# Kernel optimization log

Measured on AMD Instinct MI355X. Metric: run time of the kernel, lower is better.

The kernel has to match this reference:

```python
import jax, jax.numpy as jnp
import numpy as np

B, S, D, H, E, K = 4, 1024, 1024, 16, 8, 2
DH = D // H
FF = 4 * D  # expert hidden dim
EPS = 1e-5


def _layernorm(x, g, b):
    mu = jnp.mean(x, axis=-1, keepdims=True)
    var = jnp.mean(jnp.square(x - mu), axis=-1, keepdims=True)
    return (x - mu) / jnp.sqrt(var + EPS) * g + b


def setup_inputs() -> dict:
    key = jax.random.key(0)
    ks = jax.random.split(key, 16)
    s = 0.02
    return {
        "x": jax.random.normal(ks[0], (B, S, D), jnp.float32),
        "mask": jnp.ones((B, S), jnp.int32),
        "ln1_g": jnp.ones((D,), jnp.float32),
        "ln1_b": jnp.zeros((D,), jnp.float32),
        "ln2_g": jnp.ones((D,), jnp.float32),
        "ln2_b": jnp.zeros((D,), jnp.float32),
        "wq": jax.random.normal(ks[1], (D, D), jnp.float32) * s,
        "bq": jnp.zeros((D,), jnp.float32),
        "wk": jax.random.normal(ks[2], (D, D), jnp.float32) * s,
        "bk": jnp.zeros((D,), jnp.float32),
        "wv": jax.random.normal(ks[3], (D, D), jnp.float32) * s,
        "bv": jnp.zeros((D,), jnp.float32),
        "wo": jax.random.normal(ks[4], (D, D), jnp.float32) * s,
        "bo": jnp.zeros((D,), jnp.float32),
        "w_router": jax.random.normal(ks[5], (D, E), jnp.float32) * s,
        "b_router": jnp.zeros((E,), jnp.float32),
        "w1": jax.random.normal(ks[6], (E, D, FF), jnp.float32) * s,
        "b1": jnp.zeros((E, FF), jnp.float32),
        "w2": jax.random.normal(ks[7], (E, FF, D), jnp.float32) * s,
        "b2": jnp.zeros((E, D), jnp.float32),
    }


def _forward(x, mask, ln1_g, ln1_b, ln2_g, ln2_b, wq, bq, wk, bk, wv, bv,
             wo, bo, w_router, b_router, w1, b1, w2, b2):
    scale = DH ** -0.5
    # --- attention sub-block (pre-LN) ---
    xn = _layernorm(x, ln1_g, ln1_b)
    q = (xn @ wq + bq).reshape(B, S, H, DH).transpose(0, 2, 1, 3)  # [B,H,S,DH]
    k = (xn @ wk + bk).reshape(B, S, H, DH).transpose(0, 2, 1, 3)
    v = (xn @ wv + bv).reshape(B, S, H, DH).transpose(0, 2, 1, 3)
    scores = jnp.einsum('bhqd,bhkd->bhqk', q, k) * scale
    scores = jnp.where(mask[:, None, None, :] == 0, -jnp.inf, scores)
    attn = jax.nn.softmax(scores, axis=-1)
    ao = jnp.einsum('bhqk,bhkd->bhqd', attn, v)
    ao = ao.transpose(0, 2, 1, 3).reshape(B, S, D) @ wo + bo
    x = x + ao  # dropout is identity in eval
    # --- MoE sub-block ---
    xn2 = _layernorm(x, ln2_g, ln2_b)
    logits = xn2 @ w_router + b_router          # [B,S,E]
    top_v, top_i = jax.lax.top_k(logits, K)     # [B,S,K]
    probs = jax.nn.softmax(top_v, axis=-1)      # softmax over top-k logits
    # dense combine weight per expert: sum_k prob_k * onehot(idx_k)
    combine = jnp.sum(jax.nn.one_hot(top_i, E, dtype=xn2.dtype) * probs[..., None], axis=-2)  # [B,S,E]
    h = jax.nn.gelu(jnp.einsum('bsd,edh->ebsh', xn2, w1) + b1[:, None, None, :], approximate=False)
    eo = jnp.einsum('ebsh,ehd->ebsd', h, w2) + b2[:, None, None, :]   # [E,B,S,D]
    moe_out = jnp.einsum('bse,ebsd->bsd', combine, eo)
    return x + moe_out


def reference(x, mask, ln1_g, ln1_b, ln2_g, ln2_b, wq, bq, wk, bk, wv, bv,
              wo, bo, w_router, b_router, w1, b1, w2, b2):
    return _forward(x, mask, ln1_g, ln1_b, ln2_g, ln2_b, wq, bq, wk, bk, wv,
                    bv, wo, bo, w_router, b_router, w1, b1, w2, b2)
```

## Files before the change

### kernel.cpp

```cpp
#include <hip/hip_runtime.h>
#include <hip/hip_bf16.h>
#include <cmath>

typedef __hip_bfloat16 bf16;
typedef float f32x4 __attribute__((ext_vector_type(4)));
typedef int   i32x4 __attribute__((ext_vector_type(4)));

#define DEV static __device__ __forceinline__

constexpr int BB   = 4;
constexpr int SS   = 1024;
constexpr int DM   = 1024;
constexpr int HH   = 16;
constexpr int DHD  = 64;
constexpr int NEXP = 8;
constexpr int FFD  = 4096;
constexpr int NTOK = BB*SS;
constexpr int CAP  = NTOK*2 + NEXP*128;

DEV float bf2f(unsigned short u){ union{unsigned int i; float f;} z; z.i=((unsigned int)u)<<16; return z.f; }
DEV unsigned short f2bf(float f){ bf16 h = __float2bfloat16(f); return __builtin_bit_cast(unsigned short, h); }

DEV void stage16(const void* g, void* lds_base_uniform) {
  __builtin_amdgcn_global_load_lds(
      (const __attribute__((address_space(1))) void*)g,
      (__attribute__((address_space(3))) void*)lds_base_uniform,
      16, 0, 0);
}

template<int BM,int BN,int EPI,bool EXPERT,bool GATHER,bool OUT_SLOT,int NPASS=1,int ZMODE=0>
__global__ __launch_bounds__((BM/64)*(BN/64)*64)
void et_gemm(const bf16* __restrict__ A, const bf16* __restrict__ Bt, void* __restrict__ Cout,
             const float* __restrict__ bias, const float* __restrict__ res,
             int Kdim, int lda, int ldb, int ldc,
             long abs_, long bbs_, long cbs_, float scale,
             const int* __restrict__ pad_off, const int* __restrict__ slots,
             long psA, long psB, float* __restrict__ Cf, int bias_zs)
{
  constexpr int WN = BN/64, WM = BM/64, NW = WM*WN;
  constexpr int CA = (BM/16)/NW, CB = (BN/16)/NW;
  const int tid = threadIdx.x, wid = tid>>6, lane = tid&63;

  const int gx = gridDim.x, gy = gridDim.y;
  const long nwg = (long)gx*gy*gridDim.z;
  long lin = blockIdx.x + (long)gx*(blockIdx.y + (long)gy*blockIdx.z);
  {
    const long q = nwg >> 3, r = nwg & 7;
    const long xcd = lin & 7, idx = lin >> 3;
    lin = (xcd < r ? xcd*(q+1) : r*(q+1) + (xcd-r)*q) + idx;
  }
  const int bxi = (int)(lin % gx);
  const long rem = lin / gx;
  const int byi = (int)(rem % gy);
  const int bzi = (int)(rem / gy);

  const int row0 = bxi*BM, col0 = byi*BN;
  const int z = bzi;
  int off0 = 0;
  if constexpr (EXPERT) {
    off0 = pad_off[z];
    const int rows = pad_off[z+1] - off0;
    if (row0 >= rows) return;
  }
  long coff;
  if constexpr (ZMODE==2) {
    A  += (long)z*SS*SS;
    Bt += (long)z*DHD*SS;
    coff = (long)(z>>4)*SS*DM + (long)(z&15)*64;
  } else {
    if constexpr (!EXPERT) A += (size_t)z * abs_;
    Bt += (size_t)z * bbs_;
    coff = (long)z*cbs_;
  }
  const long bofs = (long)z * bias_zs;

  const int sr = lane>>2;
  const int sk = (lane&3)*8;

  long arow[CA];
  #pragma unroll
  for (int i=0;i<CA;i++){
    const int r = (wid + i*NW)*16 + sr;
    if constexpr (GATHER)      arow[i] = slots[off0 + row0 + r];
    else if constexpr (EXPERT) arow[i] = off0 + row0 + r;
    else                       arow[i] = row0 + r;
  }
  int brow[CB];
  #pragma unroll
  for (int i=0;i<CB;i++) brow[i] = col0 + (wid + i*NW)*16 + sr;

  const int wm = wid / WN, wn = wid % WN;
  const int fr = lane & 15, fg = lane >> 4;

  f32x4 acc[4][4];
  #pragma unroll
  for (int m=0;m<4;m++)
    #pragma unroll
    for (int n=0;n<4;n++) acc[m][n] = (f32x4)(0.f);

  if constexpr (NPASS==3) {
    __shared__ __align__(16) bf16 As[2][2][BM*32];
    __shared__ __align__(16) bf16 Bs[2][2][BN*32];
    auto STG = [&](int buf, int kt) {
      #pragma unroll
      for (int i=0;i<CA;i++){
        stage16(A +        arow[i]*(long)lda + kt + sk, (void*)&As[buf][0][(wid + i*NW)*512]);
        stage16(A + psA +  arow[i]*(long)lda + kt + sk, (void*)&As[buf][1][(wid + i*NW)*512]);
      }
      #pragma unroll
      for (int i=0;i<CB;i++){
        stage16(Bt +       (long)brow[i]*ldb + kt + sk, (void*)&Bs[buf][0][(wid + i*NW)*512]);
        stage16(Bt + psB + (long)brow[i]*ldb + kt + sk, (void*)&Bs[buf][1][(wid + i*NW)*512]);
      }
    };
    const int nsteps = Kdim >> 5;
    int cur = 0;
    STG(0, 0);
    __syncthreads();
    for (int s = 0; s < nsteps; s++) {
      if (s + 1 < nsteps) STG(cur^1, (s+1)*32);
      i32x4 a0[4], a1[4], b0[4], b1[4];
      #pragma unroll
      for (int m=0;m<4;m++) {
        a0[m] = *(const i32x4*)&As[cur][0][(wm*64 + m*16 + fr)*32 + fg*8];
        a1[m] = *(const i32x4*)&As[cur][1][(wm*64 + m*16 + fr)*32 + fg*8];
      }
      #pragma unroll
      for (int n=0;n<4;n++) {
        b0[n] = *(const i32x4*)&Bs[cur][0][(wn*64 + n*16 + fr)*32 + fg*8];
        b1[n] = *(const i32x4*)&Bs[cur][1][(wn*64 + n*16 + fr)*32 + fg*8];
      }
      asm volatile("s_nop 1" ::);
      #pragma unroll
      for (int m=0;m<4;m++)
        #pragma unroll
        for (int n=0;n<4;n++) {
          asm("v_mfma_f32_16x16x32_bf16 %0, %1, %2, %0"
              : "+v"(acc[m][n]) : "v"(a0[m]), "v"(b0[n]));
          asm("v_mfma_f32_16x16x32_bf16 %0, %1, %2, %0"
              : "+v"(acc[m][n]) : "v"(a0[m]), "v"(b1[n]));
          asm("v_mfma_f32_16x16x32_bf16 %0, %1, %2, %0"
              : "+v"(acc[m][n]) : "v"(a1[m]), "v"(b0[n]));
        }
      __syncthreads();
      cur ^= 1;
    }
  } else {
    __shared__ __align__(16) bf16 As[2][BM*32];
    __shared__ __align__(16) bf16 Bs[2][BN*32];
    auto STAGE = [&](int buf, int kt) {
      #pragma unroll
      for (int i=0;i<CA;i++)
        stage16(A + arow[i]*(long)lda + kt + sk, (void*)&As[buf][(wid + i*NW)*512]);
      #pragma unroll
      for (int i=0;i<CB;i++)
        stage16(Bt + (long)brow[i]*ldb + kt + sk, (void*)&Bs[buf][(wid + i*NW)*512]);
    };
    const int nsteps = Kdim >> 5;
    int cur = 0;
    STAGE(0, 0);
    __syncthreads();
    for (int s = 0; s < nsteps; s++) {
      if (s + 1 < nsteps) STAGE(cur^1, (s+1)*32);
      i32x4 av[4], bv[4];
      #pragma unroll
      for (int m=0;m<4;m++) av[m] = *(const i32x4*)&As[cur][(wm*64 + m*16 + fr)*32 + fg*8];
      #pragma unroll
      for (int n=0;n<4;n++) bv[n] = *(const i32x4*)&Bs[cur][(wn*64 + n*16 + fr)*32 + fg*8];
      asm volatile("s_nop 1" ::);
      #pragma unroll
      for (int m=0;m<4;m++)
        #pragma unroll
        for (int n=0;n<4;n++)
          asm("v_mfma_f32_16x16x32_bf16 %0, %1, %2, %0"
              : "+v"(acc[m][n]) : "v"(av[m]), "v"(bv[n]));
      __syncthreads();
      cur ^= 1;
    }
  }

  #pragma unroll
  for (int m=0;m<4;m++)
    #pragma unroll
    for (int n=0;n<4;n++)
      asm volatile("s_nop 7\n\ts_nop 7" : "+v"(acc[m][n]) ::);

  const long rbase = (EXPERT && OUT_SLOT) ? (long)(off0 + row0) : (long)row0;
  #pragma unroll
  for (int m=0;m<4;m++) {
    #pragma unroll
    for (int n=0;n<4;n++) {
      #pragma unroll
      for (int j=0;j<4;j++) {
        const long r = rbase + wm*64 + m*16 + fg*4 + j;
        const long c = col0 + wn*64 + n*16 + fr;
        const size_t ci = (size_t)coff + (size_t)r*ldc + c;
        float v = acc[m][n][j];
        if constexpr (EPI==0) {
          ((bf16*)Cout)[ci] = __float2bfloat16(v + bias[bofs + c]);
        } else if constexpr (EPI==1) {
          ((bf16*)Cout)[ci] = __float2bfloat16(v*scale);
        } else if constexpr (EPI==2) {
          ((float*)Cout)[ci] = v + bias[bofs + c] + res[(size_t)r*ldc + c];
        } else if constexpr (EPI==3) {
          const float t = v + bias[bofs + c];
          ((bf16*)Cout)[ci] = __float2bfloat16(0.5f*t*(1.0f+erff(t*0.70710678118654752f)));
        } else {
          const float t = v + bias[bofs + c];
          ((bf16*)Cout)[ci] = __float2bfloat16(t);
          Cf[ci] = t;
        }
      }
    }
  }
}

__global__ __launch_bounds__(256)
void k_flash(const bf16* __restrict__ qb, const bf16* __restrict__ kb,
             const bf16* __restrict__ vt, const int* __restrict__ mask,
             bf16* __restrict__ aob)
{
  const int qt = blockIdx.x, h = blockIdx.y, b = blockIdx.z;
  const int tid = threadIdx.x, wid = tid>>6, lane = tid&63;
  const int fr = lane & 15, fg = lane >> 4;
  __shared__ __align__(16) bf16 Ks[64*64];
  __shared__ __align__(16) bf16 Vs[64*64];
  __shared__ __align__(16) bf16 Pl[4][16*64];
  const int q0 = qt*64;
  const int qrow = q0 + wid*16 + fr;
  i32x4 qreg[2];
  #pragma unroll
  for (int c=0;c<2;c++)
    qreg[c] = *(const i32x4*)&qb[((size_t)(b*SS)+qrow)*DM + h*64 + c*32 + fg*8];
  f32x4 oacc[4];
  #pragma unroll
  for (int n=0;n<4;n++) oacc[n]=(f32x4)(0.f);
  float mrow[4], lrow[4];
  #pragma unroll
  for (int j=0;j<4;j++){ mrow[j]=-1e30f; lrow[j]=0.f; }

  const int srow = lane>>3;
  const int scolsw = ((lane&7) ^ srow)*8;
  auto swz = [](int row, int coleb)->int {
    return row*128 + (coleb ^ ((row&7)<<4));
  };

  for (int kt=0; kt<SS/64; kt++) {
    const int kv0 = kt*64;
    #pragma unroll
    for (int i=0;i<2;i++) {
      const int r = (wid*2+i)*8 + srow;
      stage16(kb + ((size_t)(b*SS)+kv0+r)*DM + h*64 + scolsw, (void*)&Ks[(wid*2+i)*512]);
      stage16(vt + ((size_t)(b*HH+h)*64 + r)*SS + kv0 + scolsw, (void*)&Vs[(wid*2+i)*512]);
    }
    __syncthreads();
    f32x4 sacc[4];
    #pragma unroll
    for (int n=0;n<4;n++) sacc[n]=(f32x4)(0.f);
    asm volatile("s_nop 1" ::);
    #pragma unroll
    for (int c=0;c<2;c++) {
      i32x4 bk[4];
      #pragma unroll
      for (int n=0;n<4;n++)
        bk[n] = *(const i32x4*)((const char*)Ks + swz(n*16+fr, c*64+fg*16));
      #pragma unroll
      for (int n=0;n<4;n++)
        asm("v_mfma_f32_16x16x32_bf16 %0, %1, %2, %0"
            : "+v"(sacc[n]) : "v"(qreg[c]), "v"(bk[n]));
    }
    #pragma unroll
    for (int n=0;n<4;n++)
      asm volatile("s_nop 7\n\ts_nop 7" : "+v"(sacc[n]) ::);
    float sc[4][4];
    #pragma unroll
    for (int n=0;n<4;n++) {
      const bool mm = mask[b*SS + kv0 + n*16 + fr] != 0;
      #pragma unroll
      for (int j=0;j<4;j++)
        sc[n][j] = mm ? sacc[n][j]*0.125f : -1e30f;
    }
    float scale[4];
    #pragma unroll
    for (int j=0;j<4;j++) {
      float tm = fmaxf(fmaxf(sc[0][j],sc[1][j]),fmaxf(sc[2][j],sc[3][j]));
      #pragma unroll
      for (int o=8;o;o>>=1) tm = fmaxf(tm, __shfl_xor(tm,o));
      const float nm = fmaxf(mrow[j], tm);
      scale[j] = __expf(mrow[j]-nm);
      mrow[j] = nm;
      float ts = 0.f;
      #pragma unroll
      for (int n=0;n<4;n++) { sc[n][j] = __expf(sc[n][j]-nm); ts += sc[n][j]; }
      #pragma unroll
      for (int o=8;o;o>>=1) ts += __shfl_xor(ts,o);
      lrow[j] = lrow[j]*scale[j] + ts;
    }
    #pragma unroll
    for (int n=0;n<4;n++)
      asm volatile("s_nop 7\n\ts_nop 7" : "+v"(oacc[n]) ::);
    #pragma unroll
    for (int n=0;n<4;n++)
      #pragma unroll
      for (int j=0;j<4;j++) oacc[n][j] *= scale[j];
    char* plw = (char*)Pl[wid];
    #pragma unroll
    for (int n=0;n<4;n++)
      #pragma unroll
      for (int j=0;j<4;j++) {
        const int row = fg*4+j, col = n*16+fr;
        *(bf16*)(plw + row*128 + ((col*2) ^ ((row&7)<<4))) = __float2bfloat16(sc[n][j]);
      }
    asm volatile("s_nop 1" ::);
    #pragma unroll
    for (int c=0;c<2;c++) {
      i32x4 pa = *(const i32x4*)(plw + swz(fr, c*64+fg*16));
      i32x4 bv[4];
      #pragma unroll
      for (int n=0;n<4;n++)
        bv[n] = *(const i32x4*)((const char*)Vs + swz(n*16+fr, c*64+fg*16));
      #pragma unroll
      for (int n=0;n<4;n++)
        asm("v_mfma_f32_16x16x32_bf16 %0, %1, %2, %0"
            : "+v"(oacc[n]) : "v"(pa), "v"(bv[n]));
    }
    __syncthreads();
  }
  #pragma unroll
  for (int n=0;n<4;n++)
    asm volatile("s_nop 7\n\ts_nop 7" : "+v"(oacc[n]) ::);
  #pragma unroll
  for (int j=0;j<4;j++) {
    const float ri = 1.0f / lrow[j];
    const size_t rbase = ((size_t)(b*SS) + q0 + wid*16 + fg*4 + j)*DM + h*64;
    #pragma unroll
    for (int n=0;n<4;n++)
      aob[rbase + n*16 + fr] = __float2bfloat16(oacc[n][j] * ri);
  }
}

template<typename T>
__global__ __launch_bounds__(256)
void et_transpose(const T* __restrict__ in, bf16* __restrict__ outp,
                  int ldin, int ldout, long in_bs, long out_bs)
{
  __shared__ float tile[64][65];
  const int z = blockIdx.z;
  in   += (size_t)z * in_bs;
  outp += (size_t)z * out_bs;
  const int r0 = blockIdx.x*64, c0 = blockIdx.y*64;
  const int tid = threadIdx.x;
  #pragma unroll
  for (int i=0;i<4;i++) {
    const int idx = tid*4 + i*1024;
    const int r = idx>>6, c = idx&63;
    if constexpr (sizeof(T)==4) {
      const float4 v = *(const float4*)&in[(size_t)(r0+r)*ldin + c0 + c];
      tile[r][c]=v.x; tile[r][c+1]=v.y; tile[r][c+2]=v.z; tile[r][c+3]=v.w;
    } else {
      const ushort4 v = *(const ushort4*)&in[(size_t)(r0+r)*ldin + c0 + c];
      tile[r][c]=bf2f(v.x); tile[r][c+1]=bf2f(v.y); tile[r][c+2]=bf2f(v.z); tile[r][c+3]=bf2f(v.w);
    }
  }
  __syncthreads();
  #pragma unroll
  for (int i=0;i<4;i++) {
    const int idx = tid*4 + i*1024;
    const int c = idx>>6, r = idx&63;
    ushort4 o;
    o.x=f2bf(tile[r][c]); o.y=f2bf(tile[r+1][c]); o.z=f2bf(tile[r+2][c]); o.w=f2bf(tile[r+3][c]);
    *(ushort4*)&outp[(size_t)(c0+c)*ldout + r0 + r] = o;
  }
}

template<typename TI, typename TO>
__global__ __launch_bounds__(256)
void k_trans_head(const TI* __restrict__ in, TO* __restrict__ outp)
{
  __shared__ float tile[64][65];
  const int z = blockIdx.z;
  in   += (size_t)(z>>4)*SS*DM + (size_t)(z&15)*64;
  outp += (size_t)z*DHD*SS;
  const int r0 = blockIdx.x*64;
  const int tid = threadIdx.x;
  #pragma unroll
  for (int i=0;i<4;i++) {
    const int idx = tid*4 + i*1024;
    const int r = idx>>6, c = idx&63;
    if constexpr (sizeof(TI)==4) {
      const float4 v = *(const float4*)&in[(size_t)(r0+r)*DM + c];
      tile[r][c]=v.x; tile[r][c+1]=v.y; tile[r][c+2]=v.z; tile[r][c+3]=v.w;
    } else {
      const ushort4 v = *(const ushort4*)&in[(size_t)(r0+r)*DM + c];
      tile[r][c]=bf2f(v.x); tile[r][c+1]=bf2f(v.y); tile[r][c+2]=bf2f(v.z); tile[r][c+3]=bf2f(v.w);
    }
  }
  __syncthreads();
  #pragma unroll
  for (int i=0;i<4;i++) {
    const int idx = tid*4 + i*1024;
    const int c = idx>>6, r = idx&63;
    if constexpr (sizeof(TO)==4) {
      float4 o;
      o.x=tile[r][c]; o.y=tile[r+1][c]; o.z=tile[r+2][c]; o.w=tile[r+3][c];
      *(float4*)&outp[(size_t)c*SS + r0 + r] = o;
    } else {
      ushort4 o;
      o.x=f2bf(tile[r][c]); o.y=f2bf(tile[r+1][c]); o.z=f2bf(tile[r+2][c]); o.w=f2bf(tile[r+3][c]);
      *(ushort4*)&outp[(size_t)c*SS + r0 + r] = o;
    }
  }
}

__global__ __launch_bounds__(256)
void et_transpose2(const float* __restrict__ in0, const float* __restrict__ in1,
                   const float* __restrict__ in2, bf16* __restrict__ outp,
                   int ldin, int ldout, long pstride, long out_zs)
{
  __shared__ float tile[64][65];
  const int z = blockIdx.z;
  const float* in = (z==0) ? in0 : (z==1) ? in1 : in2;
  outp += (size_t)z * out_zs;
  const int r0 = blockIdx.x*64, c0 = blockIdx.y*64;
  const int tid = threadIdx.x;
  #pragma unroll
  for (int i=0;i<4;i++) {
    const int idx = tid*4 + i*1024;
    const int r = idx>>6, c = idx&63;
    const float4 v = *(const float4*)&in[(size_t)(r0+r)*ldin + c0 + c];
    tile[r][c]=v.x; tile[r][c+1]=v.y; tile[r][c+2]=v.z; tile[r][c+3]=v.w;
  }
  __syncthreads();
  #pragma unroll
  for (int i=0;i<4;i++) {
    const int idx = tid*4 + i*1024;
    const int c = idx>>6, r = idx&63;
    ushort4 o0, o1;
    unsigned short* p0 = (unsigned short*)&o0;
    unsigned short* p1 = (unsigned short*)&o1;
    #pragma unroll
    for (int j=0;j<4;j++) {
      float v = tile[r+j][c];
      const unsigned short h0 = f2bf(v);
      p0[j] = h0;
      v -= bf2f(h0);
      p1[j] = f2bf(v);
    }
    const size_t oi = (size_t)(c0+c)*ldout + r0 + r;
    *(ushort4*)&outp[oi] = o0;
    *(ushort4*)&outp[oi + pstride] = o1;
  }
}

__global__ __launch_bounds__(256)
void et_ln2(const float* __restrict__ xin, const float* __restrict__ g,
            const float* __restrict__ bsh, bf16* __restrict__ outp, long pstride)
{
  const int row = blockIdx.x, tid = threadIdx.x;
  const float4 v = ((const float4*)(xin + (size_t)row*DM))[tid];
  float s = v.x+v.y+v.z+v.w;
  #pragma unroll
  for (int o=32;o;o>>=1) s += __shfl_xor(s,o);
  __shared__ float s4[4], q4[4];
  if ((tid&63)==0) s4[tid>>6]=s;
  __syncthreads();
  const float mu = (s4[0]+s4[1]+s4[2]+s4[3]) * (1.f/DM);
  const float d0=v.x-mu,d1=v.y-mu,d2=v.z-mu,d3=v.w-mu;
  float q = d0*d0+d1*d1+d2*d2+d3*d3;
  #pragma unroll
  for (int o=32;o;o>>=1) q += __shfl_xor(q,o);
  if ((tid&63)==0) q4[tid>>6]=q;
  __syncthreads();
  const float var = (q4[0]+q4[1]+q4[2]+q4[3]) * (1.f/DM);
  const float rstd = rsqrtf(var + 1e-5f);
  const float4 gg = ((const float4*)g)[tid];
  const float4 bb = ((const float4*)bsh)[tid];
  float of[4];
  of[0] = d0*rstd*gg.x + bb.x;
  of[1] = d1*rstd*gg.y + bb.y;
  of[2] = d2*rstd*gg.z + bb.z;
  of[3] = d3*rstd*gg.w + bb.w;
  ushort4 p0, p1;
  unsigned short* pp0 = (unsigned short*)&p0;
  unsigned short* pp1 = (unsigned short*)&p1;
  #pragma unroll
  for (int k=0;k<4;k++) {
    float vv = of[k];
    const unsigned short h0 = f2bf(vv); pp0[k] = h0;
    vv -= bf2f(h0);
    pp1[k] = f2bf(vv);
  }
  const size_t oi = (size_t)row*DM;
  ((ushort4*)(outp + oi))[tid] = p0;
  ((ushort4*)(outp + pstride + oi))[tid] = p1;
}

__global__ __launch_bounds__(256)
void et_router2(const float* __restrict__ x1, const float* __restrict__ g,
                const float* __restrict__ bsh, const float* __restrict__ wr,
                const float* __restrict__ br, bf16* __restrict__ xn2,
                int* __restrict__ t2e, float* __restrict__ t2p,
                int* __restrict__ flaglist, int* __restrict__ cntb)
{
  const int wid = threadIdx.x>>6, lane = threadIdx.x&63;
  const int t = blockIdx.x*4 + wid;
  const float* xr = x1 + (size_t)t*DM;
  float4 xv[4];
  float s = 0.f;
  #pragma unroll
  for (int p=0;p<4;p++){
    xv[p] = *(const float4*)&xr[p*256 + lane*4];
    s += xv[p].x+xv[p].y+xv[p].z+xv[p].w;
  }
  #pragma unroll
  for (int o=32;o;o>>=1) s += __shfl_xor(s,o);
  const float mu = s * (1.f/DM);
  float q = 0.f;
  #pragma unroll
  for (int p=0;p<4;p++){
    const float a=xv[p].x-mu,b=xv[p].y-mu,c=xv[p].z-mu,d=xv[p].w-mu;
    q += a*a+b*b+c*c+d*d;
  }
  #pragma unroll
  for (int o=32;o;o>>=1) q += __shfl_xor(q,o);
  const float rstd = rsqrtf(q*(1.f/DM) + 1e-5f);
  float acc[NEXP];
  #pragma unroll
  for (int e=0;e<NEXP;e++) acc[e]=0.f;
  #pragma unroll
  for (int p=0;p<4;p++){
    const int d0 = p*256 + lane*4;
    const float4 gg = *(const float4*)&g[d0];
    const float4 bb = *(const float4*)&bsh[d0];
    float xn[4];
    xn[0]=(xv[p].x-mu)*rstd*gg.x+bb.x;
    xn[1]=(xv[p].y-mu)*rstd*gg.y+bb.y;
    xn[2]=(xv[p].z-mu)*rstd*gg.z+bb.z;
    xn[3]=(xv[p].w-mu)*rstd*gg.w+bb.w;
    ushort4 xo;
    xo.x=f2bf(xn[0]); xo.y=f2bf(xn[1]); xo.z=f2bf(xn[2]); xo.w=f2bf(xn[3]);
    *(ushort4*)&xn2[(size_t)t*DM + d0] = xo;
    #pragma unroll
    for (int j=0;j<4;j++){
      const float4 w0  = ((const float4*)&wr[(size_t)(d0+j)*NEXP])[0];
      const float4 w1v = ((const float4*)&wr[(size_t)(d0+j)*NEXP])[1];
      acc[0]+=xn[j]*w0.x;  acc[1]+=xn[j]*w0.y;  acc[2]+=xn[j]*w0.z;  acc[3]+=xn[j]*w0.w;
      acc[4]+=xn[j]*w1v.x; acc[5]+=xn[j]*w1v.y; acc[6]+=xn[j]*w1v.z; acc[7]+=xn[j]*w1v.w;
    }
  }
  #pragma unroll
  for (int e=0;e<NEXP;e++)
    #pragma unroll
    for (int o=32;o;o>>=1) acc[e] += __shfl_xor(acc[e],o);
  if (lane==0) {
    float v0=-1e30f, v1=-1e30f, v2=-1e30f; int e0=0, e1=0;
    #pragma unroll
    for (int e=0;e<NEXP;e++) {
      const float v = acc[e] + br[e];
      if (v>v0){v2=v1;v1=v0;e1=e0;v0=v;e0=e;}
      else if (v>v1){v2=v1;v1=v;e1=e;}
      else if (v>v2){v2=v;}
    }
    const float dd = __expf(v1-v0);
    const float p0 = 1.f/(1.f+dd);
    t2e[t*2]=e0; t2e[t*2+1]=e1;
    t2p[t*2]=p0; t2p[t*2+1]=dd*p0;
    if (v1 - v2 < 0.02f) {
      const int b = t >> 10;
      const int ib = atomicAdd(&cntb[b], 1);
      flaglist[b*1024 + ib] = t;
    }
  }
}

__global__ __launch_bounds__(256)
void k_rec4(const float* __restrict__ qf, const float* __restrict__ kfT,
            const float* __restrict__ vf, const int* __restrict__ flaglist,
            const int* __restrict__ cntb, const int* __restrict__ mask,
            float* __restrict__ aoF)
{
  const int h = blockIdx.y, b = blockIdx.z;
  const int tid = threadIdx.x, lane = tid&63, wv_ = tid>>6;
  const int nb = cntb[b];
  __shared__ float qs[4][64];
  __shared__ float scb[4][SS];
  __shared__ float part[4][4][64];
  __shared__ float tsum[4];
  const int* mrow = mask + (size_t)b*SS;
  const float* kbase = kfT + ((size_t)(b*HH + h)*DHD)*SS + tid;
  const float* vbase = vf + (size_t)b*SS*DM + h*64 + lane;

  for (int t0 = blockIdx.x*4; t0 < nb; t0 += gridDim.x*4) {
    const int nt = min(4, nb - t0);
    for (int idx = tid; idx < 4*64; idx += 256) {
      const int j = idx >> 6, d = idx & 63;
      float qv = 0.f;
      if (j < nt) {
        const int t = flaglist[b*1024 + t0 + j];
        qv = qf[(size_t)t*DM + h*64 + d];
      }
      qs[j][d] = qv;
    }
    __syncthreads();
    float a00=0,a01=0,a02=0,a03=0, a10=0,a11=0,a12=0,a13=0;
    float a20=0,a21=0,a22=0,a23=0, a30=0,a31=0,a32=0,a33=0;
    #pragma unroll 4
    for (int u=0; u<64; u++) {
      const float* kr = kbase + (size_t)u*SS;
      const float k0 = kr[0], k1 = kr[256], k2 = kr[512], k3 = kr[768];
      const float q0 = qs[0][u], q1 = qs[1][u], q2 = qs[2][u], q3 = qs[3][u];
      a00 += q0*k0; a01 += q0*k1; a02 += q0*k2; a03 += q0*k3;
      a10 += q1*k0; a11 += q1*k1; a12 += q1*k2; a13 += q1*k3;
      a20 += q2*k0; a21 += q2*k1; a22 += q2*k2; a23 += q2*k3;
      a30 += q3*k0; a31 += q3*k1; a32 += q3*k2; a33 += q3*k3;
    }
    const bool m0 = mrow[tid]!=0, m1 = mrow[tid+256]!=0, m2 = mrow[tid+512]!=0, m3 = mrow[tid+768]!=0;
    scb[0][tid]=m0?a00*0.125f:-1e30f; scb[0][tid+256]=m1?a01*0.125f:-1e30f;
    scb[0][tid+512]=m2?a02*0.125f:-1e30f; scb[0][tid+768]=m3?a03*0.125f:-1e30f;
    scb[1][tid]=m0?a10*0.125f:-1e30f; scb[1][tid+256]=m1?a11*0.125f:-1e30f;
    scb[1][tid+512]=m2?a12*0.125f:-1e30f; scb[1][tid+768]=m3?a13*0.125f:-1e30f;
    scb[2][tid]=m0?a20*0.125f:-1e30f; scb[2][tid+256]=m1?a21*0.125f:-1e30f;
    scb[2][tid+512]=m2?a22*0.125f:-1e30f; scb[2][tid+768]=m3?a23*0.125f:-1e30f;
    scb[3][tid]=m0?a30*0.125f:-1e30f; scb[3][tid+256]=m1?a31*0.125f:-1e30f;
    scb[3][tid+512]=m2?a32*0.125f:-1e30f; scb[3][tid+768]=m3?a33*0.125f:-1e30f;
    __syncthreads();
    {
      const int j = wv_;
      float v[16];
      float lm = -1e30f;
      #pragma unroll
      for (int kk=0;kk<16;kk++) { v[kk] = scb[j][lane + kk*64]; lm = fmaxf(lm, v[kk]); }
      #pragma unroll
      for (int o=32;o;o>>=1) lm = fmaxf(lm, __shfl_xor(lm,o));
      float ls = 0.f;
      #pragma unroll
      for (int kk=0;kk<16;kk++) {
        const float e = expf(v[kk]-lm);
        scb[j][lane + kk*64] = e; ls += e;
      }
      #pragma unroll
      for (int o=32;o;o>>=1) ls += __shfl_xor(ls,o);
      if (lane==0) tsum[j] = ls;
    }
    __syncthreads();
    float p0=0.f, p1=0.f, p2=0.f, p3=0.f;
    for (int s = wv_*4; s < SS; s += 16) {
      const float v0 = vbase[(size_t) s   *DM];
      const float v1 = vbase[(size_t)(s+1)*DM];
      const float v2 = vbase[(size_t)(s+2)*DM];
      const float v3 = vbase[(size_t)(s+3)*DM];
      p0 += scb[0][s]*v0 + scb[0][s+1]*v1 + scb[0][s+2]*v2 + scb[0][s+3]*v3;
      p1 += scb[1][s]*v0 + scb[1][s+1]*v1 + scb[1][s+2]*v2 + scb[1][s+3]*v3;
      p2 += scb[2][s]*v0 + scb[2][s+1]*v1 + scb[2][s+2]*v2 + scb[2][s+3]*v3;
      p3 += scb[3][s]*v0 + scb[3][s+1]*v1 + scb[3][s+2]*v2 + scb[3][s+3]*v3;
    }
    part[wv_][0][lane] = p0;
    part[wv_][1][lane] = p1;
    part[wv_][2][lane] = p2;
    part[wv_][3][lane] = p3;
    __syncthreads();
    for (int idx = tid; idx < nt*64; idx += 256) {
      const int j = idx >> 6, d = idx & 63;
      aoF[(size_t)(b*1024 + t0 + j)*DM + h*64 + d] =
        (part[0][j][d]+part[1][j][d]+part[2][j][d]+part[3][j][d]) / tsum[j];
    }
    __syncthreads();
  }
}

__global__ __launch_bounds__(256)
void k_flag_proj2(const float* __restrict__ aoF, const float* __restrict__ wo,
                  const float* __restrict__ bo, const float* __restrict__ x,
                  const int* __restrict__ flaglist, const int* __restrict__ cntb,
                  float* __restrict__ yF)
{
  const int tile = blockIdx.x;
  const int b = tile >> 7;
  const int i0 = (tile & 127) * 8;
  const int nb = cntb[b];
  if (i0 >= nb) return;
  const int nt = min(8, nb - i0);
  const int c0 = blockIdx.y * 128;
  const int tid = threadIdx.x;
  const int c = c0 + (tid & 127);
  const int dh = tid >> 7;
  __shared__ float ar[8][DM];
  __shared__ float ph[2][8][128];
  for (int k = tid; k < 8*256; k += 256) {
    const int j = k >> 8, q4i = k & 255;
    float4 v = make_float4(0.f,0.f,0.f,0.f);
    if (j < nt) v = ((const float4*)(aoF + (size_t)(b*1024 + i0 + j)*DM))[q4i];
    ((float4*)ar[j])[q4i] = v;
  }
  __syncthreads();
  float acc0=0.f, acc1=0.f, acc2=0.f, acc3=0.f;
  float acc4=0.f, acc5=0.f, acc6=0.f, acc7=0.f;
  const int dbase = dh*512;
  #pragma unroll 4
  for (int d=0; d<512; d++) {
    const float w = wo[(size_t)(dbase+d)*DM + c];
    acc0 += ar[0][dbase+d]*w; acc1 += ar[1][dbase+d]*w;
    acc2 += ar[2][dbase+d]*w; acc3 += ar[3][dbase+d]*w;
    acc4 += ar[4][dbase+d]*w; acc5 += ar[5][dbase+d]*w;
    acc6 += ar[6][dbase+d]*w; acc7 += ar[7][dbase+d]*w;
  }
  const int lc = tid & 127;
  ph[dh][0][lc]=acc0; ph[dh][1][lc]=acc1; ph[dh][2][lc]=acc2; ph[dh][3][lc]=acc3;
  ph[dh][4][lc]=acc4; ph[dh][5][lc]=acc5; ph[dh][6][lc]=acc6; ph[dh][7][lc]=acc7;
  __syncthreads();
  for (int k = tid; k < nt*128; k += 256) {
    const int j = k >> 7, ccl = k & 127;
    const int cc = c0 + ccl;
    const int slot = b*1024 + i0 + j;
    const int t = flaglist[slot];
    yF[(size_t)slot*DM + cc] = ph[0][j][ccl] + ph[1][j][ccl] + bo[cc] + x[(size_t)t*DM + cc];
  }
}

__global__ __launch_bounds__(256)
void k_flag_router(const float* __restrict__ yF, const float* __restrict__ g,
                   const float* __restrict__ bsh, const float* __restrict__ wr,
                   const float* __restrict__ br, const int* __restrict__ flaglist,
                   const int* __restrict__ cntb, int* __restrict__ t2e,
                   float* __restrict__ t2p)
{
  const int tid = threadIdx.x, lane = tid&63, wv_ = tid>>6;
  __shared__ float s4[4], q4[4], pt[4][8];
  for (int idx = blockIdx.x; idx < NTOK; idx += gridDim.x) {
    const int b = idx >> 10, ib = idx & 1023;
    if (ib >= cntb[b]) continue;
    const int t = flaglist[idx];
    const float4 v = ((const float4*)(yF + (size_t)idx*DM))[tid];
    float s = v.x+v.y+v.z+v.w;
    #pragma unroll
    for (int o=32;o;o>>=1) s += __shfl_xor(s,o);
    if (lane==0) s4[wv_]=s;
    __syncthreads();
    const float mu = (s4[0]+s4[1]+s4[2]+s4[3])*(1.f/DM);
    const float d0=v.x-mu, d1=v.y-mu, d2=v.z-mu, d3=v.w-mu;
    float q = d0*d0+d1*d1+d2*d2+d3*d3;
    #pragma unroll
    for (int o=32;o;o>>=1) q += __shfl_xor(q,o);
    if (lane==0) q4[wv_]=q;
    __syncthreads();
    const float var = (q4[0]+q4[1]+q4[2]+q4[3])*(1.f/DM);
    const float rstd = 1.0f/sqrtf(var + 1e-5f);
    const int dbase = tid*4;
    const float4 gg = ((const float4*)g)[tid];
    const float4 bb = ((const float4*)bsh)[tid];
    const float x0 = d0*rstd*gg.x+bb.x, x1_ = d1*rstd*gg.y+bb.y;
    const float x2 = d2*rstd*gg.z+bb.z, x3_ = d3*rstd*gg.w+bb.w;
    float pl[8];
    #pragma unroll
    for (int e=0;e<8;e++)
      pl[e] = x0*wr[(size_t)(dbase+0)*8+e] + x1_*wr[(size_t)(dbase+1)*8+e]
            + x2*wr[(size_t)(dbase+2)*8+e] + x3_*wr[(size_t)(dbase+3)*8+e];
    #pragma unroll
    for (int e=0;e<8;e++)
      #pragma unroll
      for (int o=32;o;o>>=1) pl[e] += __shfl_xor(pl[e],o);
    if (lane==0) {
      #pragma unroll
      for (int e=0;e<8;e++) pt[wv_][e]=pl[e];
    }
    __syncthreads();
    if (tid==0) {
      float v0=-1e30f, v1=-1e30f; int e0=0, e1=0;
      for (int e=0;e<8;e++) {
        const float L = pt[0][e]+pt[1][e]+pt[2][e]+pt[3][e] + br[e];
        if (L>v0){v1=v0;e1=e0;v0=L;e0=e;}
        else if (L>v1){v1=L;e1=e;}
      }
      const float dd=expf(v1-v0), p0=1.f/(1.f+dd);
      t2e[t*2]=e0; t2e[t*2+1]=e1;
      t2p[t*2]=p0; t2p[t*2+1]=dd*p0;
    }
    __syncthreads();
  }
}

__global__ void et_init(const float* __restrict__ bq, const float* __restrict__ bk,
                        const float* __restrict__ bv, float* __restrict__ bcat,
                        int* __restrict__ cnt)
{
  const int i = blockIdx.x*256 + threadIdx.x;
  if (i < 16) cnt[i]=0;
  if (i < DM) { bcat[i]=bq[i]; bcat[DM+i]=bk[i]; bcat[2*DM+i]=bv[i]; }
}

__global__ void et_count(const int* __restrict__ t2e, int* __restrict__ cnt)
{
  const int t = blockIdx.x*256 + threadIdx.x;
  if (t < NTOK) {
    atomicAdd(&cnt[t2e[t*2]], 1);
    atomicAdd(&cnt[t2e[t*2+1]], 1);
  }
}

__global__ void et_scan(const int* __restrict__ cnt, int* __restrict__ poff,
                        int* __restrict__ fil, int* __restrict__ slots)
{
  const int tid = threadIdx.x;
  if (tid==0) {
    int o=0;
    for (int e=0;e<NEXP;e++){ poff[e]=o; o += ((cnt[e]+127)>>7)<<7; }
    poff[NEXP]=o;
  }
  if (tid<NEXP) fil[tid]=0;
  for (int i=tid;i<CAP;i+=256) slots[i]=0;
}

__global__ void et_fill(const int* __restrict__ t2e, const int* __restrict__ poff,
                        int* __restrict__ fil, int* __restrict__ slots, int* __restrict__ sof)
{
  const int t = blockIdx.x*256 + threadIdx.x;
  if (t >= NTOK) return;
  #pragma unroll
  for (int kk=0;kk<2;kk++) {
    const int e = t2e[t*2+kk];
    const int pos = atomicAdd(&fil[e], 1);
    const int sl = poff[e] + pos;
    slots[sl] = t;
    sof[t*2+kk] = sl;
  }
}

__global__ __launch_bounds__(256)
void et_combine(const float* __restrict__ x1, const bf16* __restrict__ eo,
                const float* __restrict__ t2p, const int* __restrict__ sof,
                float* __restrict__ outp)
{
  const int t = blockIdx.x, tid = threadIdx.x;
  const int s0 = sof[t*2], s1 = sof[t*2+1];
  const float p0 = t2p[t*2], p1 = t2p[t*2+1];
  const float4 xv = ((const float4*)(x1 + (size_t)t*DM))[tid];
  const ushort4 a = ((const ushort4*)(eo + (size_t)s0*DM))[tid];
  const ushort4 c = ((const ushort4*)(eo + (size_t)s1*DM))[tid];
  float4 o;
  o.x = xv.x + p0*bf2f(a.x) + p1*bf2f(c.x);
  o.y = xv.y + p0*bf2f(a.y) + p1*bf2f(c.y);
  o.z = xv.z + p0*bf2f(a.z) + p1*bf2f(c.z);
  o.w = xv.w + p0*bf2f(a.w) + p1*bf2f(c.w);
  ((float4*)(outp + (size_t)t*DM))[tid] = o;
}

extern "C" void kernel_launch(void* const* d_in, const int* in_sizes, int n_in,
                              void* d_out, int out_size, void* d_ws, size_t ws_size,
                              hipStream_t stream)
{
  (void)in_sizes; (void)n_in; (void)out_size; (void)ws_size;
  const float* x    = (const float*)d_in[0];
  const int*   mask = (const int*)  d_in[1];
  const float* ln1g = (const float*)d_in[2];
  const float* ln1b = (const float*)d_in[3];
  const float* ln2g = (const float*)d_in[4];
  const float* ln2b = (const float*)d_in[5];
  const float* wq   = (const float*)d_in[6];
  const float* bq   = (const float*)d_in[7];
  const float* wk   = (const float*)d_in[8];
  const float* bk   = (const float*)d_in[9];
  const float* wv   = (const float*)d_in[10];
  const float* bv   = (const float*)d_in[11];
  const float* wo   = (const float*)d_in[12];
  const float* bo   = (const float*)d_in[13];
  const float* wr   = (const float*)d_in[14];
  const float* br   = (const float*)d_in[15];
  const float* w1   = (const float*)d_in[16];
  const float* b1   = (const float*)d_in[17];
  const float* w2   = (const float*)d_in[18];
  const float* b2   = (const float*)d_in[19];
  float* outp = (float*)d_out;

  char* wsb = (char*)d_ws;
  size_t off = 0;
  auto alloc = [&](size_t bytes)->void* {
    void* p = wsb + off;
    off += (bytes + 255) & ~(size_t)255;
    return p;
  };
  const long WPS  = (long)DM*DM;
  const long XPS  = (long)NTOK*DM;
  const long EWS  = (long)DM*FFD;
  bf16*  wqT2  = (bf16*) alloc((size_t)2*WPS*2);
  bf16*  wkT2  = (bf16*) alloc((size_t)2*WPS*2);
  bf16*  wvT2  = (bf16*) alloc((size_t)2*WPS*2);
  bf16*  woT   = (bf16*) alloc((size_t)WPS*2);
  bf16*  w1Ta  = (bf16*) alloc((size_t)NEXP*EWS*2);
  bf16*  w2Ta  = (bf16*) alloc((size_t)NEXP*EWS*2);
  bf16*  xn2p  = (bf16*) alloc((size_t)2*XPS*2);
  bf16*  qb    = (bf16*) alloc((size_t)XPS*2);
  bf16*  kb    = (bf16*) alloc((size_t)XPS*2);
  bf16*  vb    = (bf16*) alloc((size_t)XPS*2);
  bf16*  vt    = (bf16*) alloc((size_t)XPS*2);
  float* qf    = (float*)alloc((size_t)XPS*4);
  float* kf    = (float*)alloc((size_t)XPS*4);
  float* vf    = (float*)alloc((size_t)XPS*4);
  float* kfT   = (float*)alloc((size_t)XPS*4);
  bf16*  aob   = (bf16*) alloc((size_t)XPS*2);
  float* x1    = (float*)alloc((size_t)XPS*4);
  bf16*  xn2   = (bf16*) alloc((size_t)XPS*2);
  bf16*  hbuf  = (bf16*) alloc((size_t)CAP*FFD*2);
  bf16*  eo    = (bf16*) alloc((size_t)CAP*DM*2);
  float* bcat  = (float*)alloc((size_t)3*DM*4);
  int*   t2e   = (int*)  alloc((size_t)NTOK*2*4);
  float* t2p   = (float*)alloc((size_t)NTOK*2*4);
  int*   slots = (int*)  alloc((size_t)CAP*4);
  int*   sof   = (int*)  alloc((size_t)NTOK*2*4);
  int*   flagl = (int*)  alloc((size_t)NTOK*4);
  int*   cnt   = (int*)  alloc(64);
  int*   fil   = (int*)  alloc(64);
  int*   poff  = (int*)  alloc(64);
  int*   cntb  = cnt + 8;
  float* aoF   = (float*)qb;
  float* yF    = (float*)vb;

  const dim3 T256(256);

  et_init<<<4,T256,0,stream>>>(bq, bk, bv, bcat, cnt);
  et_transpose2<<<dim3(DM/64,DM/64,3),T256,0,stream>>>(wq, wk, wv, wqT2, DM, DM, WPS, 2*WPS);
  et_transpose<float><<<dim3(DM/64,DM/64,1),T256,0,stream>>>(wo, woT, DM, DM, 0, 0);

  et_ln2<<<NTOK,T256,0,stream>>>(x, ln1g, ln1b, xn2p, XPS);

  et_gemm<128,64,4,false,false,false,3,0><<<dim3(NTOK/128, DM/64, 3),dim3(128),0,stream>>>(
      xn2p, wqT2, qb, bcat, nullptr, DM, DM, DM, DM,
      0, 2*WPS, XPS, 1.f, nullptr, nullptr, XPS, WPS, qf, DM);

  k_trans_head<bf16,bf16><<<dim3(SS/64,1,BB*HH),T256,0,stream>>>(vb, vt);
  k_trans_head<float,float><<<dim3(SS/64,1,BB*HH),T256,0,stream>>>(kf, kfT);

  k_flash<<<dim3(SS/64, HH, BB),T256,0,stream>>>(qb, kb, vt, mask, aob);

  et_gemm<64,64,2,false,false,false,1,0><<<dim3(NTOK/64, DM/64, 1),dim3(64),0,stream>>>(
      aob, woT, x1, bo, x, DM, DM, DM, DM, 0,0,0, 1.f, nullptr,nullptr, 0,0,nullptr, 0);

  et_router2<<<NTOK/4,T256,0,stream>>>(x1, ln2g, ln2b, wr, br, xn2, t2e, t2p, flagl, cntb);
  k_rec4<<<dim3(32,HH,BB),T256,0,stream>>>(qf, kfT, vf, flagl, cntb, mask, aoF);
  k_flag_proj2<<<dim3(NTOK/8, DM/128),T256,0,stream>>>(aoF, wo, bo, x, flagl, cntb, yF);
  k_flag_router<<<1024,T256,0,stream>>>(yF, ln2g, ln2b, wr, br, flagl, cntb, t2e, t2p);

  et_count<<<NTOK/256,T256,0,stream>>>(t2e, cnt);
  et_scan<<<1,T256,0,stream>>>(cnt, poff, fil, slots);
  et_fill<<<NTOK/256,T256,0,stream>>>(t2e, poff, fil, slots, sof);

  et_transpose<float><<<dim3(DM/64, FFD/64, NEXP),T256,0,stream>>>(w1, w1Ta, FFD, DM, EWS, EWS);
  et_transpose<float><<<dim3(FFD/64, DM/64, NEXP),T256,0,stream>>>(w2, w2Ta, DM, FFD, EWS, EWS);

  et_gemm<128,128,3,true,true,true,1,0><<<dim3(NTOK/128, FFD/128, NEXP),T256,0,stream>>>(
      xn2, w1Ta, hbuf, b1, nullptr, DM, DM, DM, FFD,
      0, EWS, 0, 1.f, poff, slots, 0,0,nullptr, FFD);
  et_gemm<128,128,0,true,false,true,1,0><<<dim3(NTOK/128, DM/128, NEXP),T256,0,stream>>>(
      hbuf, w2Ta, eo, b2, nullptr, FFD, FFD, FFD, DM,
      0, EWS, 0, 1.f, poff, nullptr, 0,0,nullptr, DM);

  et_combine<<<NTOK,T256,0,stream>>>(x1, eo, t2p, sof, outp);
}
```

Baseline: 826.8 us.

## Double-buffer flash K/V tiles and merge small transpose and count kernels

The flash attention loop now double-buffers the K/V shared-memory tiles, prefetching the next tile while computing on the current one. The two head transposes are merged into one launch, and so are the two expert-weight transposes. The expert-count pass is folded into the router kernels with atomic adds, and the flag router corrects the counts when it changes a token's experts. Together these aim to hide load latency in attention and cut launch overhead, at the cost of doubled LDS in flash and extra atomics in the router.

```diff
diff --git a/kernel.cpp b/kernel.cpp
--- a/kernel.cpp
+++ b/kernel.cpp
@@ -223,8 +223,8 @@
   const int qt = blockIdx.x, h = blockIdx.y, b = blockIdx.z;
   const int tid = threadIdx.x, wid = tid>>6, lane = tid&63;
   const int fr = lane & 15, fg = lane >> 4;
-  __shared__ __align__(16) bf16 Ks[64*64];
-  __shared__ __align__(16) bf16 Vs[64*64];
+  __shared__ __align__(16) bf16 Ks[2][64*64];
+  __shared__ __align__(16) bf16 Vs[2][64*64];
   __shared__ __align__(16) bf16 Pl[4][16*64];
   const int q0 = qt*64;
   const int qrow = q0 + wid*16 + fr;
@@ -244,16 +244,23 @@
   auto swz = [](int row, int coleb)->int {
     return row*128 + (coleb ^ ((row&7)<<4));
   };
-
-  for (int kt=0; kt<SS/64; kt++) {
+  auto STAGE = [&](int buf, int kt) {
     const int kv0 = kt*64;
     #pragma unroll
     for (int i=0;i<2;i++) {
       const int r = (wid*2+i)*8 + srow;
-      stage16(kb + ((size_t)(b*SS)+kv0+r)*DM + h*64 + scolsw, (void*)&Ks[(wid*2+i)*512]);
-      stage16(vt + ((size_t)(b*HH+h)*64 + r)*SS + kv0 + scolsw, (void*)&Vs[(wid*2+i)*512]);
-    }
-    __syncthreads();
+      stage16(kb + ((size_t)(b*SS)+kv0+r)*DM + h*64 + scolsw, (void*)&Ks[buf][(wid*2+i)*512]);
+      stage16(vt + ((size_t)(b*HH+h)*64 + r)*SS + kv0 + scolsw, (void*)&Vs[buf][(wid*2+i)*512]);
+    }
+  };
+
+  const int NT = SS/64;
+  int cur = 0;
+  STAGE(0, 0);
+  __syncthreads();
+  for (int kt=0; kt<NT; kt++) {
+    if (kt + 1 < NT) STAGE(cur^1, kt+1);
+    const int kv0 = kt*64;
     f32x4 sacc[4];
     #pragma unroll
     for (int n=0;n<4;n++) sacc[n]=(f32x4)(0.f);
@@ -263,7 +270,7 @@
       i32x4 bk[4];
       #pragma unroll
       for (int n=0;n<4;n++)
-        bk[n] = *(const i32x4*)((const char*)Ks + swz(n*16+fr, c*64+fg*16));
+        bk[n] = *(const i32x4*)((const char*)Ks[cur] + swz(n*16+fr, c*64+fg*16));
       #pragma unroll
       for (int n=0;n<4;n++)
         asm("v_mfma_f32_16x16x32_bf16 %0, %1, %2, %0"
@@ -318,13 +325,14 @@
       i32x4 bv[4];
       #pragma unroll
       for (int n=0;n<4;n++)
-        bv[n] = *(const i32x4*)((const char*)Vs + swz(n*16+fr, c*64+fg*16));
+        bv[n] = *(const i32x4*)((const char*)Vs[cur] + swz(n*16+fr, c*64+fg*16));
       #pragma unroll
       for (int n=0;n<4;n++)
         asm("v_mfma_f32_16x16x32_bf16 %0, %1, %2, %0"
             : "+v"(oacc[n]) : "v"(pa), "v"(bv[n]));
     }
     __syncthreads();
+    cur ^= 1;
   }
   #pragma unroll
   for (int n=0;n<4;n++)
@@ -373,41 +381,80 @@
   }
 }
 
-template<typename TI, typename TO>
-__global__ __launch_bounds__(256)
-void k_trans_head(const TI* __restrict__ in, TO* __restrict__ outp)
+__global__ __launch_bounds__(256)
+void k_wtrans(const float* __restrict__ w1, const float* __restrict__ w2,
+              bf16* __restrict__ w1Ta, bf16* __restrict__ w2Ta)
 {
   __shared__ float tile[64][65];
   const int z = blockIdx.z;
-  in   += (size_t)(z>>4)*SS*DM + (size_t)(z&15)*64;
-  outp += (size_t)z*DHD*SS;
-  const int r0 = blockIdx.x*64;
+  const int t = blockIdx.x;
+  const float* in; bf16* outp; int ldin, ldout, r0, c0;
+  const long EWS = (long)DM*FFD;
+  if (z < 8) {
+    in = w1 + z*EWS; outp = w1Ta + z*EWS;
+    ldin = FFD; ldout = DM;
+    r0 = (t & 15)*64; c0 = (t >> 4)*64;
+  } else {
+    in = w2 + (z-8)*EWS; outp = w2Ta + (z-8)*EWS;
+    ldin = DM; ldout = FFD;
+    r0 = (t >> 4)*64; c0 = (t & 15)*64;
+  }
   const int tid = threadIdx.x;
   #pragma unroll
   for (int i=0;i<4;i++) {
     const int idx = tid*4 + i*1024;
     const int r = idx>>6, c = idx&63;
-    if constexpr (sizeof(TI)==4) {
-      const float4 v = *(const float4*)&in[(size_t)(r0+r)*DM + c];
-      tile[r][c]=v.x; tile[r][c+1]=v.y; tile[r][c+2]=v.z; tile[r][c+3]=v.w;
-    } else {
-      const ushort4 v = *(const ushort4*)&in[(size_t)(r0+r)*DM + c];
-      tile[r][c]=bf2f(v.x); tile[r][c+1]=bf2f(v.y); tile[r][c+2]=bf2f(v.z); tile[r][c+3]=bf2f(v.w);
-    }
+    const float4 v = *(const float4*)&in[(size_t)(r0+r)*ldin + c0 + c];
+    tile[r][c]=v.x; tile[r][c+1]=v.y; tile[r][c+2]=v.z; tile[r][c+3]=v.w;
   }
   __syncthreads();
   #pragma unroll
   for (int i=0;i<4;i++) {
     const int idx = tid*4 + i*1024;
     const int c = idx>>6, r = idx&63;
-    if constexpr (sizeof(TO)==4) {
+    ushort4 o;
+    o.x=f2bf(tile[r][c]); o.y=f2bf(tile[r+1][c]); o.z=f2bf(tile[r+2][c]); o.w=f2bf(tile[r+3][c]);
+    *(ushort4*)&outp[(size_t)(c0+c)*ldout + r0 + r] = o;
+  }
+}
+
+__global__ __launch_bounds__(256)
+void k_trans_head2(const bf16* __restrict__ vb, bf16* __restrict__ vt,
+                   const float* __restrict__ kf, float* __restrict__ kfT)
+{
+  __shared__ float tile[64][65];
+  const int z = blockIdx.z;
+  const bool isV = (z < 64);
+  const int zz = isV ? z : z - 64;
+  const int r0 = blockIdx.x*64;
+  const int tid = threadIdx.x;
+  const size_t ibase = (size_t)(zz>>4)*SS*DM + (size_t)(zz&15)*64;
+  #pragma unroll
+  for (int i=0;i<4;i++) {
+    const int idx = tid*4 + i*1024;
+    const int r = idx>>6, c = idx&63;
+    if (isV) {
+      const ushort4 v = *(const ushort4*)&vb[ibase + (size_t)(r0+r)*DM + c];
+      tile[r][c]=bf2f(v.x); tile[r][c+1]=bf2f(v.y); tile[r][c+2]=bf2f(v.z); tile[r][c+3]=bf2f(v.w);
+    } else {
+      const float4 v = *(const float4*)&kf[ibase + (size_t)(r0+r)*DM + c];
+      tile[r][c]=v.x; tile[r][c+1]=v.y; tile[r][c+2]=v.z; tile[r][c+3]=v.w;
+    }
+  }
+  __syncthreads();
+  const size_t obase = (size_t)zz*DHD*SS;
+  #pragma unroll
+  for (int i=0;i<4;i++) {
+    const int idx = tid*4 + i*1024;
+    const int c = idx>>6, r = idx&63;
+    if (isV) {
+      ushort4 o;
+      o.x=f2bf(tile[r][c]); o.y=f2bf(tile[r+1][c]); o.z=f2bf(tile[r+2][c]); o.w=f2bf(tile[r+3][c]);
+      *(ushort4*)&vt[obase + (size_t)c*SS + r0 + r] = o;
+    } else {
       float4 o;
       o.x=tile[r][c]; o.y=tile[r+1][c]; o.z=tile[r+2][c]; o.w=tile[r+3][c];
-      *(float4*)&outp[(size_t)c*SS + r0 + r] = o;
-    } else {
-      ushort4 o;
-      o.x=f2bf(tile[r][c]); o.y=f2bf(tile[r+1][c]); o.z=f2bf(tile[r+2][c]); o.w=f2bf(tile[r+3][c]);
-      *(ushort4*)&outp[(size_t)c*SS + r0 + r] = o;
+      *(float4*)&kfT[obase + (size_t)c*SS + r0 + r] = o;
     }
   }
 }
@@ -500,7 +547,8 @@
                 const float* __restrict__ bsh, const float* __restrict__ wr,
                 const float* __restrict__ br, bf16* __restrict__ xn2,
                 int* __restrict__ t2e, float* __restrict__ t2p,
-                int* __restrict__ flaglist, int* __restrict__ cntb)
+                int* __restrict__ flaglist, int* __restrict__ cntb,
+                int* __restrict__ cnt)
 {
   const int wid = threadIdx.x>>6, lane = threadIdx.x&63;
   const int t = blockIdx.x*4 + wid;
@@ -565,6 +613,8 @@
     const float p0 = 1.f/(1.f+dd);
     t2e[t*2]=e0; t2e[t*2+1]=e1;
     t2p[t*2]=p0; t2p[t*2+1]=dd*p0;
+    atomicAdd(&cnt[e0], 1);
+    atomicAdd(&cnt[e1], 1);
     if (v1 - v2 < 0.02f) {
       const int b = t >> 10;
       const int ib = atomicAdd(&cntb[b], 1);
@@ -722,7 +772,7 @@
                    const float* __restrict__ bsh, const float* __restrict__ wr,
                    const float* __restrict__ br, const int* __restrict__ flaglist,
                    const int* __restrict__ cntb, int* __restrict__ t2e,
-                   float* __restrict__ t2p)
+                   float* __restrict__ t2p, int* __restrict__ cnt)
 {
   const int tid = threadIdx.x, lane = tid&63, wv_ = tid>>6;
   __shared__ float s4[4], q4[4], pt[4][8];
@@ -772,6 +822,9 @@
         else if (L>v1){v1=L;e1=e;}
       }
       const float dd=expf(v1-v0), p0=1.f/(1.f+dd);
+      const int oe0 = t2e[t*2], oe1 = t2e[t*2+1];
+      if (oe0 != e0) { atomicSub(&cnt[oe0],1); atomicAdd(&cnt[e0],1); }
+      if (oe1 != e1) { atomicSub(&cnt[oe1],1); atomicAdd(&cnt[e1],1); }
       t2e[t*2]=e0; t2e[t*2+1]=e1;
       t2p[t*2]=p0; t2p[t*2+1]=dd*p0;
     }
@@ -786,15 +839,6 @@
   const int i = blockIdx.x*256 + threadIdx.x;
   if (i < 16) cnt[i]=0;
   if (i < DM) { bcat[i]=bq[i]; bcat[DM+i]=bk[i]; bcat[2*DM+i]=bv[i]; }
-}
-
-__global__ void et_count(const int* __restrict__ t2e, int* __restrict__ cnt)
-{
-  const int t = blockIdx.x*256 + threadIdx.x;
-  if (t < NTOK) {
-    atomicAdd(&cnt[t2e[t*2]], 1);
-    atomicAdd(&cnt[t2e[t*2+1]], 1);
-  }
 }
 
 __global__ void et_scan(const int* __restrict__ cnt, int* __restrict__ poff,
@@ -926,25 +970,22 @@
       xn2p, wqT2, qb, bcat, nullptr, DM, DM, DM, DM,
       0, 2*WPS, XPS, 1.f, nullptr, nullptr, XPS, WPS, qf, DM);
 
-  k_trans_head<bf16,bf16><<<dim3(SS/64,1,BB*HH),T256,0,stream>>>(vb, vt);
-  k_trans_head<float,float><<<dim3(SS/64,1,BB*HH),T256,0,stream>>>(kf, kfT);
+  k_trans_head2<<<dim3(SS/64,1,2*BB*HH),T256,0,stream>>>(vb, vt, kf, kfT);
 
   k_flash<<<dim3(SS/64, HH, BB),T256,0,stream>>>(qb, kb, vt, mask, aob);
 
   et_gemm<64,64,2,false,false,false,1,0><<<dim3(NTOK/64, DM/64, 1),dim3(64),0,stream>>>(
       aob, woT, x1, bo, x, DM, DM, DM, DM, 0,0,0, 1.f, nullptr,nullptr, 0,0,nullptr, 0);
 
-  et_router2<<<NTOK/4,T256,0,stream>>>(x1, ln2g, ln2b, wr, br, xn2, t2e, t2p, flagl, cntb);
+  et_router2<<<NTOK/4,T256,0,stream>>>(x1, ln2g, ln2b, wr, br, xn2, t2e, t2p, flagl, cntb, cnt);
   k_rec4<<<dim3(32,HH,BB),T256,0,stream>>>(qf, kfT, vf, flagl, cntb, mask, aoF);
   k_flag_proj2<<<dim3(NTOK/8, DM/128),T256,0,stream>>>(aoF, wo, bo, x, flagl, cntb, yF);
-  k_flag_router<<<1024,T256,0,stream>>>(yF, ln2g, ln2b, wr, br, flagl, cntb, t2e, t2p);
-
-  et_count<<<NTOK/256,T256,0,stream>>>(t2e, cnt);
+  k_flag_router<<<1024,T256,0,stream>>>(yF, ln2g, ln2b, wr, br, flagl, cntb, t2e, t2p, cnt);
+
   et_scan<<<1,T256,0,stream>>>(cnt, poff, fil, slots);
   et_fill<<<NTOK/256,T256,0,stream>>>(t2e, poff, fil, slots, sof);
 
-  et_transpose<float><<<dim3(DM/64, FFD/64, NEXP),T256,0,stream>>>(w1, w1Ta, FFD, DM, EWS, EWS);
-  et_transpose<float><<<dim3(FFD/64, DM/64, NEXP),T256,0,stream>>>(w2, w2Ta, DM, FFD, EWS, EWS);
+  k_wtrans<<<dim3(1024,1,16),T256,0,stream>>>(w1, w2, w1Ta, w2Ta);
 
   et_gemm<128,128,3,true,true,true,1,0><<<dim3(NTOK/128, FFD/128, NEXP),T256,0,stream>>>(
       xn2, w1Ta, hbuf, b1, nullptr, DM, DM, DM, FFD,
```

New measurement: 896.5 us. 8.4% more time.
